# Performance work log

Hardware: AMD Instinct MI355X
Metric: run time of the kernel (lower is better)

The kernel has to match this reference:

```python
import jax, jax.numpy as jnp
import numpy as np


def _rot_mat(thetas, scales):
    # thetas, scales: [bs, g] -> [bs, g, 9, 9] bilinear-interpolation matrices
    bs, g = thetas.shape
    t = thetas.reshape(-1)
    s = scales.reshape(-1)
    x = jnp.cos(t) * s
    y = jnp.sin(t) * s
    yp = -y
    z = jnp.zeros_like(x)
    o = jnp.ones_like(x)
    a = x - y; b = x * y; c = x + y; d = a * c; e = a + c
    ap = x - yp; bp = x * yp; cp = x + yp; dp = ap * cp; ep = ap + cp

    def M(rows):
        # rows: 9 lists of 9 [N]-arrays -> [9, 9, N]
        return jnp.stack([jnp.stack(r, axis=0) for r in rows], axis=0)

    ctr = [z, z, z, z, o, z, z, z, z]

    pb1 = M([
        [a, 1 - a, z, z, z, z, z, z, z],
        [z, 1 - y, y, z, z, z, z, z, z],
        [z, z, a, z, z, 1 - a, z, z, z],
        [y, z, z, 1 - y, z, z, z, z, z],
        ctr,
        [z, z, z, z, z, 1 - y, z, z, y],
        [z, z, z, 1 - a, z, z, a, z, z],
        [z, z, z, z, z, z, y, 1 - y, z],
        [z, z, z, z, z, z, z, 1 - a, a]])
    pb2 = M([
        [a, 1 - a, z, z, z, z, z, z, z],
        [z, x - b, b, z, 1 - c + b, y - b, z, z, z],
        [z, z, a, z, z, 1 - a, z, z, z],
        [b, y - b, z, x - b, 1 - c + b, z, z, z, z],
        ctr,
        [z, z, z, z, 1 - c + b, x - b, z, y - b, b],
        [z, z, z, 1 - a, z, z, a, z, z],
        [z, z, z, y - b, 1 - c + b, z, b, x - b, z],
        [z, z, z, z, z, z, z, 1 - a, a]])
    ps1 = M([
        [d, a - d, z, c - d, 1 - e + d, z, z, z, z],
        [z, x - b, b, z, 1 - c + b, y - b, z, z, z],
        [z, c - d, d, z, 1 - e + d, a - d, z, z, z],
        [b, y - b, z, x - b, 1 - c + b, z, z, z, z],
        ctr,
        [z, z, z, z, 1 - c + b, x - b, z, y - b, b],
        [z, z, z, a - d, 1 - e + d, z, d, c - d, z],
        [z, z, z, y - b, 1 - c + b, z, b, x - b, z],
        [z, z, z, z, 1 - e + d, c - d, z, a - d, d]])
    ps2 = pb2  # identical in the source
    nb1 = M([
        [cp, z, z, 1 - cp, z, z, z, z, z],
        [yp, 1 - yp, z, z, z, z, z, z, z],
        [z, 1 - cp, cp, z, z, z, z, z, z],
        [z, z, z, 1 - yp, z, z, yp, z, z],
        ctr,
        [z, z, yp, z, z, 1 - yp, z, z, z],
        [z, z, z, z, z, z, cp, 1 - cp, z],
        [z, z, z, z, z, z, z, 1 - yp, yp],
        [z, z, z, z, z, 1 - cp, z, z, cp]])
    nb2 = M([
        [cp, z, z, 1 - cp, z, z, z, z, z],
        [bp, x - bp, z, yp - bp, 1 - cp + bp, z, z, z, z],
        [z, 1 - cp, cp, z, z, z, z, z, z],
        [z, z, z, x - bp, 1 - cp + bp, z, bp, yp - bp, z],
        ctr,
        [z, yp - bp, bp, z, 1 - cp + bp, x - bp, z, z, z],
        [z, z, z, z, z, z, cp, 1 - cp, z],
        [z, z, z, z, 1 - cp + bp, yp - bp, z, x - bp, bp],
        [z, z, z, z, z, 1 - cp, z, z, cp]])
    ns1 = M([
        [dp, cp - dp, z, ap - dp, 1 - ep + dp, z, z, z, z],
        [bp, x - bp, z, yp - bp, 1 - cp + bp, z, z, z, z],
        [z, ap - dp, dp, z, 1 - ep + dp, cp - dp, z, z, z],
        [z, yp - bp, bp, z, 1 - cp + bp, x - bp, z, z, z],
        ctr,
        [z, z, z, x - bp, 1 - cp + bp, z, bp, yp - bp, z],
        [z, z, z, cp - dp, 1 - ep + dp, z, dp, ap - dp, z],
        [z, z, z, z, 1 - cp + bp, yp - bp, z, x - bp, bp],
        [z, z, z, z, 1 - ep + dp, ap - dp, z, cp - dp, dp]])
    ns2 = nb2  # mirrors the positive branch where small_2 == big_2

    m_pos = (t >= 0.0)[None, None, :]
    m_big = (s >= 1.0)[None, None, :]
    m_1 = (jnp.abs(t) <= jnp.pi / 4)[None, None, :]
    pos = jnp.where(m_big, jnp.where(m_1, pb1, pb2), jnp.where(m_1, ps1, ps2))
    neg = jnp.where(m_big, jnp.where(m_1, nb1, nb2), jnp.where(m_1, ns1, ns2))
    rot = jnp.where(m_pos, pos, neg)  # [9, 9, bs*g]
    return jnp.transpose(rot, (2, 0, 1)).reshape(bs, g, 9, 9)


def _forward(x, thetas, scales, lambdas, weight):
    # x: [B, Cin, H, W]; weight: [n, Cout, Cin, 3, 3]; thetas/scales/lambdas: [B, n]
    B, Cin, H, W = x.shape
    n, Cout = weight.shape[0], weight.shape[1]
    rot = _rot_mat(thetas, scales) * lambdas[:, :, None, None]  # [B, n, 9, 9]
    w9 = weight.reshape(n, Cout, Cin, 9)
    # per-sample transformed kernel: sum over kernel_number n and source taps j
    w = jnp.einsum('bnij,nocj->bioc', rot, w9)  # [B, 9, Cout, Cin]
    w = jnp.transpose(w, (0, 2, 3, 1)).reshape(B * Cout, Cin, 3, 3)
    xg = x.reshape(1, B * Cin, H, W)
    out = jax.lax.conv_general_dilated(
        xg, w, window_strides=(1, 1), padding=((1, 1), (1, 1)),
        dimension_numbers=('NCHW', 'OIHW', 'NCHW'), feature_group_count=B)
    return out.reshape(B, Cout, H, W)


def setup_inputs() -> dict:
    key = jax.random.key(0)
    ks = jax.random.split(key, 5)
    B, Cin, Cout, H, W, n = 16, 256, 256, 64, 64, 4
    x = jax.random.normal(ks[0], (B, Cin, H, W), dtype=jnp.float32)
    thetas = jax.random.uniform(ks[1], (B, n), minval=-1.2, maxval=1.2, dtype=jnp.float32)
    scales = jax.random.uniform(ks[2], (B, n), minval=0.5, maxval=1.5, dtype=jnp.float32)
    lambdas = jax.nn.softmax(jax.random.normal(ks[3], (B, n), dtype=jnp.float32), axis=-1)
    weight = jax.random.normal(ks[4], (n, Cout, Cin, 3, 3), dtype=jnp.float32) * 0.05
    return {"x": x, "thetas": thetas, "scales": scales, "lambdas": lambdas, "weight": weight}


def reference(x, thetas, scales, lambdas, weight):
    return _forward(x, thetas, scales, lambdas, weight)
```

## Files before the change

### kernel.cpp

```cpp
#include <hip/hip_runtime.h>
#include <cstdint>
#include <cstddef>

typedef unsigned short ushort_t;
typedef __attribute__((ext_vector_type(4))) float f32x4;
typedef __attribute__((ext_vector_type(8))) short s16x8;

#define PI_4F 0.78539816339744830962f

__device__ inline ushort_t f2bf(float f) {
  unsigned int u = __float_as_uint(f);
  u = u + 0x7fffu + ((u >> 16) & 1u);
  return (ushort_t)(u >> 16);
}

__global__ void rot_kernel(const float* __restrict__ thetas, const float* __restrict__ scales,
                           const float* __restrict__ lambdas, float* __restrict__ rot) {
  int tid = threadIdx.x;
  float t = thetas[tid], s = scales[tid], lam = lambdas[tid];
  float xv = cosf(t) * s, yv = sinf(t) * s;
  bool pos = (t >= 0.0f), big = (s >= 1.0f), m1 = (fabsf(t) <= PI_4F);
  float M[81];
#pragma unroll
  for (int i = 0; i < 81; ++i) M[i] = 0.0f;
  M[36 + 4] = 1.0f;
  if (pos) {
    float a = xv - yv, bb = xv * yv, c = xv + yv;
    if (m1 && big) {
      M[0] = a; M[1] = 1 - a;
      M[9 + 1] = 1 - yv; M[9 + 2] = yv;
      M[18 + 2] = a; M[18 + 5] = 1 - a;
      M[27 + 0] = yv; M[27 + 3] = 1 - yv;
      M[45 + 5] = 1 - yv; M[45 + 8] = yv;
      M[54 + 3] = 1 - a; M[54 + 6] = a;
      M[63 + 6] = yv; M[63 + 7] = 1 - yv;
      M[72 + 7] = 1 - a; M[72 + 8] = a;
    } else if (m1) {
      float d = a * c, e = a + c;
      M[0] = d; M[1] = a - d; M[3] = c - d; M[4] = 1 - e + d;
      M[9 + 1] = xv - bb; M[9 + 2] = bb; M[9 + 4] = 1 - c + bb; M[9 + 5] = yv - bb;
      M[18 + 1] = c - d; M[18 + 2] = d; M[18 + 4] = 1 - e + d; M[18 + 5] = a - d;
      M[27 + 0] = bb; M[27 + 1] = yv - bb; M[27 + 3] = xv - bb; M[27 + 4] = 1 - c + bb;
      M[45 + 4] = 1 - c + bb; M[45 + 5] = xv - bb; M[45 + 7] = yv - bb; M[45 + 8] = bb;
      M[54 + 3] = a - d; M[54 + 4] = 1 - e + d; M[54 + 6] = d; M[54 + 7] = c - d;
      M[63 + 3] = yv - bb; M[63 + 4] = 1 - c + bb; M[63 + 6] = bb; M[63 + 7] = xv - bb;
      M[72 + 4] = 1 - e + d; M[72 + 5] = c - d; M[72 + 7] = a - d; M[72 + 8] = d;
    } else {
      M[0] = a; M[1] = 1 - a;
      M[9 + 1] = xv - bb; M[9 + 2] = bb; M[9 + 4] = 1 - c + bb; M[9 + 5] = yv - bb;
      M[18 + 2] = a; M[18 + 5] = 1 - a;
      M[27 + 0] = bb; M[27 + 1] = yv - bb; M[27 + 3] = xv - bb; M[27 + 4] = 1 - c + bb;
      M[45 + 4] = 1 - c + bb; M[45 + 5] = xv - bb; M[45 + 7] = yv - bb; M[45 + 8] = bb;
      M[54 + 3] = 1 - a; M[54 + 6] = a;
      M[63 + 3] = yv - bb; M[63 + 4] = 1 - c + bb; M[63 + 6] = bb; M[63 + 7] = xv - bb;
      M[72 + 7] = 1 - a; M[72 + 8] = a;
    }
  } else {
    float yp = -yv;
    float ap = xv - yp, bp = xv * yp, cp = xv + yp;
    if (m1 && big) {
      M[0] = cp; M[3] = 1 - cp;
      M[9 + 0] = yp; M[9 + 1] = 1 - yp;
      M[18 + 1] = 1 - cp; M[18 + 2] = cp;
      M[27 + 3] = 1 - yp; M[27 + 6] = yp;
      M[45 + 2] = yp; M[45 + 5] = 1 - yp;
      M[54 + 6] = cp; M[54 + 7] = 1 - cp;
      M[63 + 7] = 1 - yp; M[63 + 8] = yp;
      M[72 + 5] = 1 - cp; M[72 + 8] = cp;
    } else if (m1) {
      float dp = ap * cp, ep = ap + cp;
      M[0] = dp; M[1] = cp - dp; M[3] = ap - dp; M[4] = 1 - ep + dp;
      M[9 + 0] = bp; M[9 + 1] = xv - bp; M[9 + 3] = yp - bp; M[9 + 4] = 1 - cp + bp;
      M[18 + 1] = ap - dp; M[18 + 2] = dp; M[18 + 4] = 1 - ep + dp; M[18 + 5] = cp - dp;
      M[27 + 1] = yp - bp; M[27 + 2] = bp; M[27 + 4] = 1 - cp + bp; M[27 + 5] = xv - bp;
      M[45 + 3] = xv - bp; M[45 + 4] = 1 - cp + bp; M[45 + 6] = bp; M[45 + 7] = yp - bp;
      M[54 + 3] = cp - dp; M[54 + 4] = 1 - ep + dp; M[54 + 6] = dp; M[54 + 7] = ap - dp;
      M[63 + 4] = 1 - cp + bp; M[63 + 5] = yp - bp; M[63 + 7] = xv - bp; M[63 + 8] = bp;
      M[72 + 4] = 1 - ep + dp; M[72 + 5] = ap - dp; M[72 + 7] = cp - dp; M[72 + 8] = dp;
    } else {
      M[0] = cp; M[3] = 1 - cp;
      M[9 + 0] = bp; M[9 + 1] = xv - bp; M[9 + 3] = yp - bp; M[9 + 4] = 1 - cp + bp;
      M[18 + 1] = 1 - cp; M[18 + 2] = cp;
      M[27 + 3] = xv - bp; M[27 + 4] = 1 - cp + bp; M[27 + 6] = bp; M[27 + 7] = yp - bp;
      M[45 + 1] = yp - bp; M[45 + 2] = bp; M[45 + 4] = 1 - cp + bp; M[45 + 5] = xv - bp;
      M[54 + 6] = cp; M[54 + 7] = 1 - cp;
      M[63 + 4] = 1 - cp + bp; M[63 + 5] = yp - bp; M[63 + 7] = xv - bp; M[63 + 8] = bp;
      M[72 + 5] = 1 - cp; M[72 + 8] = cp;
    }
  }
  float* r = rot + tid * 81;
#pragma unroll
  for (int i = 0; i < 81; ++i) r[i] = M[i] * lam;
}

__global__ void wt_kernel(const float* __restrict__ weight, const float* __restrict__ rot,
                          ushort_t* __restrict__ wtout) {
  __shared__ float rs[64 * 81];
  const int o = blockIdx.x;
  const int c = threadIdx.x;
  for (int i = threadIdx.x; i < 64 * 81; i += 256) rs[i] = rot[i];
  float wv[4][9];
#pragma unroll
  for (int n = 0; n < 4; ++n) {
    const float* wp = weight + (((size_t)(n * 256 + o)) * 256 + c) * 9;
#pragma unroll
    for (int j = 0; j < 9; ++j) wv[n][j] = wp[j];
  }
  __syncthreads();
  for (int b = 0; b < 16; ++b) {
#pragma unroll
    for (int i = 0; i < 9; ++i) {
      float acc = 0.0f;
#pragma unroll
      for (int n = 0; n < 4; ++n) {
        const float* r = &rs[(b * 4 + n) * 81 + i * 9];
#pragma unroll
        for (int j = 0; j < 9; ++j) acc = fmaf(r[j], wv[n][j], acc);
      }
      wtout[((size_t)((b * 9 + i) * 256 + o)) * 256 + c] = f2bf(acc);
    }
  }
}

__global__ void fill_zero(uint4* __restrict__ p) {
  p[(size_t)blockIdx.x * 256 + threadIdx.x] = make_uint4(0u, 0u, 0u, 0u);
}

__global__ void transpose_kernel(const float* __restrict__ x, ushort_t* __restrict__ xpad) {
  __shared__ float tile[32][33];
  const int b = blockIdx.z, ct = blockIdx.y, st = blockIdx.x;
  const int tx = threadIdx.x & 31, ty = threadIdx.x >> 5;
  const int hw0 = st * 32, c0 = ct * 32;
  const float* xb = x + ((size_t)(b * 256 + c0)) * 4096 + hw0;
#pragma unroll
  for (int j = 0; j < 4; ++j)
    tile[ty + j * 8][tx] = xb[(size_t)(ty + j * 8) * 4096 + tx];
  __syncthreads();
#pragma unroll
  for (int j = 0; j < 4; ++j) {
    int s = ty + j * 8;
    int hw = hw0 + s;
    int h = hw >> 6, w = hw & 63;
    xpad[((size_t)(b * 4356 + (h + 1) * 66 + (w + 1))) * 256 + c0 + tx] = f2bf(tile[tx][s]);
  }
}

__device__ inline void gload16(const ushort_t* g, ushort_t* l) {
  __builtin_amdgcn_global_load_lds(
      (const __attribute__((address_space(1))) unsigned int*)g,
      (__attribute__((address_space(3))) unsigned int*)l, 16, 0, 0);
}

__global__ void conv_kernel(const ushort_t* __restrict__ xpad, const ushort_t* __restrict__ wt,
                            float* __restrict__ out) {
  __shared__ __align__(16) ushort_t As[128 * 32];
  __shared__ __align__(16) ushort_t Bs[128 * 32];
  const int ntile = blockIdx.x;
  const int mtile = blockIdx.y;
  const int b = blockIdx.z;
  const int t = threadIdx.x;
  const int wave = t >> 6, lane = t & 63;
  const int wm = wave & 1, wn = wave >> 1;
  const int lr = lane & 15, lq = lane >> 4;
  const int o0 = mtile * 128, h0 = ntile * 2;

  const ushort_t* wt_b = wt + (size_t)b * 589824;
  const ushort_t* xp_b = xpad + (size_t)b * 1115136;

  const int lrow = t >> 2;
  const int lco = (t & 3) * 8;

  ushort_t* As0 = As + wave * 512;
  ushort_t* As1 = As + 2048 + wave * 512;
  ushort_t* Bs0 = Bs + wave * 512;
  ushort_t* Bs1 = Bs + 2048 + wave * 512;

  f32x4 acc[4][4];
#pragma unroll
  for (int i = 0; i < 4; ++i)
#pragma unroll
    for (int j = 0; j < 4; ++j) acc[i][j] = (f32x4)(0.0f);

  for (int ks = 0; ks < 72; ++ks) {
    const int tap = ks >> 3;
    const int c0 = (ks & 7) << 5;
    const int kh = tap / 3, kw = tap - kh * 3;

    __syncthreads();
    {
      const ushort_t* ga = wt_b + ((size_t)(tap * 256 + o0 + lrow)) * 256 + c0 + lco;
      gload16(ga, As0);
      gload16(ga + 64 * 256, As1);
      const int sp0 = (h0 + kh) * 66 + lrow + kw;
      const ushort_t* gb = xp_b + (size_t)sp0 * 256 + c0 + lco;
      gload16(gb, Bs0);
      gload16(gb + 66 * 256, Bs1);
    }
    asm volatile("s_waitcnt vmcnt(0)" ::: "memory");
    __syncthreads();

    s16x8 af[4], bfr[4];
#pragma unroll
    for (int mi = 0; mi < 4; ++mi)
      af[mi] = *(const s16x8*)(As + ((wm * 64 + mi * 16 + lr) * 32 + lq * 8));
#pragma unroll
    for (int ni = 0; ni < 4; ++ni)
      bfr[ni] = *(const s16x8*)(Bs + ((wn * 64 + ni * 16 + lr) * 32 + lq * 8));
#pragma unroll
    for (int mi = 0; mi < 4; ++mi)
#pragma unroll
      for (int ni = 0; ni < 4; ++ni)
        acc[mi][ni] = __builtin_amdgcn_mfma_f32_16x16x32_bf16(af[mi], bfr[ni], acc[mi][ni], 0, 0, 0);
  }

  float* ob = out + ((size_t)(b * 256 + o0 + wm * 64)) * 4096 + ntile * 128 + wn * 64 + lr;
#pragma unroll
  for (int mi = 0; mi < 4; ++mi)
#pragma unroll
    for (int r = 0; r < 4; ++r) {
      float* orow = ob + (size_t)(mi * 16 + lq * 4 + r) * 4096;
#pragma unroll
      for (int ni = 0; ni < 4; ++ni) orow[ni * 16] = acc[mi][ni][r];
    }
}

extern "C" void kernel_launch(void* const* d_in, const int* in_sizes, int n_in,
                              void* d_out, int out_size, void* d_ws, size_t ws_size,
                              hipStream_t stream) {
  const float* x = (const float*)d_in[0];
  const float* thetas = (const float*)d_in[1];
  const float* scales = (const float*)d_in[2];
  const float* lambdas = (const float*)d_in[3];
  const float* weight = (const float*)d_in[4];
  float* out = (float*)d_out;

  float* rot_ws = (float*)d_ws;
  ushort_t* wt_ws = (ushort_t*)((char*)d_ws + 32768);
  ushort_t* xpad_ws = (ushort_t*)((char*)d_ws + 32768 + 18874368);

  rot_kernel<<<1, 64, 0, stream>>>(thetas, scales, lambdas, rot_ws);
  wt_kernel<<<256, 256, 0, stream>>>(weight, rot_ws, wt_ws);
  fill_zero<<<8712, 256, 0, stream>>>((uint4*)xpad_ws);
  transpose_kernel<<<dim3(128, 8, 16), 256, 0, stream>>>(x, xpad_ws);
  conv_kernel<<<dim3(32, 2, 16), 256, 0, stream>>>(xpad_ws, wt_ws, out);
}
```

Before: 256.3 us.

## Double-buffer conv LDS, swizzle layout, remap blocks per XCD, fuse rot, zero only borders

The conv kernel now double-buffers its LDS tiles, issuing the next k-step's global-to-LDS loads before the current step's MFMAs, and adds an XOR swizzle on the 16-byte column groups to cut LDS bank conflicts. Blocks are remapped onto a 1D grid so each XCD handles a contiguous group of batch/mtile pairs for L2 locality, and launch bounds are added. The rotation-matrix computation is folded into the weight-transform kernel, which removes one launch at the cost of recomputing it in every block. The full padded-buffer memset is replaced with a kernel that zeroes only the border pixels.

```diff
diff --git a/kernel.cpp b/kernel.cpp
--- a/kernel.cpp
+++ b/kernel.cpp
@@ -14,91 +14,91 @@
   return (ushort_t)(u >> 16);
 }
 
-__global__ void rot_kernel(const float* __restrict__ thetas, const float* __restrict__ scales,
-                           const float* __restrict__ lambdas, float* __restrict__ rot) {
-  int tid = threadIdx.x;
-  float t = thetas[tid], s = scales[tid], lam = lambdas[tid];
-  float xv = cosf(t) * s, yv = sinf(t) * s;
-  bool pos = (t >= 0.0f), big = (s >= 1.0f), m1 = (fabsf(t) <= PI_4F);
-  float M[81];
-#pragma unroll
-  for (int i = 0; i < 81; ++i) M[i] = 0.0f;
-  M[36 + 4] = 1.0f;
-  if (pos) {
-    float a = xv - yv, bb = xv * yv, c = xv + yv;
-    if (m1 && big) {
-      M[0] = a; M[1] = 1 - a;
-      M[9 + 1] = 1 - yv; M[9 + 2] = yv;
-      M[18 + 2] = a; M[18 + 5] = 1 - a;
-      M[27 + 0] = yv; M[27 + 3] = 1 - yv;
-      M[45 + 5] = 1 - yv; M[45 + 8] = yv;
-      M[54 + 3] = 1 - a; M[54 + 6] = a;
-      M[63 + 6] = yv; M[63 + 7] = 1 - yv;
-      M[72 + 7] = 1 - a; M[72 + 8] = a;
-    } else if (m1) {
-      float d = a * c, e = a + c;
-      M[0] = d; M[1] = a - d; M[3] = c - d; M[4] = 1 - e + d;
-      M[9 + 1] = xv - bb; M[9 + 2] = bb; M[9 + 4] = 1 - c + bb; M[9 + 5] = yv - bb;
-      M[18 + 1] = c - d; M[18 + 2] = d; M[18 + 4] = 1 - e + d; M[18 + 5] = a - d;
-      M[27 + 0] = bb; M[27 + 1] = yv - bb; M[27 + 3] = xv - bb; M[27 + 4] = 1 - c + bb;
-      M[45 + 4] = 1 - c + bb; M[45 + 5] = xv - bb; M[45 + 7] = yv - bb; M[45 + 8] = bb;
-      M[54 + 3] = a - d; M[54 + 4] = 1 - e + d; M[54 + 6] = d; M[54 + 7] = c - d;
-      M[63 + 3] = yv - bb; M[63 + 4] = 1 - c + bb; M[63 + 6] = bb; M[63 + 7] = xv - bb;
-      M[72 + 4] = 1 - e + d; M[72 + 5] = c - d; M[72 + 7] = a - d; M[72 + 8] = d;
-    } else {
-      M[0] = a; M[1] = 1 - a;
-      M[9 + 1] = xv - bb; M[9 + 2] = bb; M[9 + 4] = 1 - c + bb; M[9 + 5] = yv - bb;
-      M[18 + 2] = a; M[18 + 5] = 1 - a;
-      M[27 + 0] = bb; M[27 + 1] = yv - bb; M[27 + 3] = xv - bb; M[27 + 4] = 1 - c + bb;
-      M[45 + 4] = 1 - c + bb; M[45 + 5] = xv - bb; M[45 + 7] = yv - bb; M[45 + 8] = bb;
-      M[54 + 3] = 1 - a; M[54 + 6] = a;
-      M[63 + 3] = yv - bb; M[63 + 4] = 1 - c + bb; M[63 + 6] = bb; M[63 + 7] = xv - bb;
-      M[72 + 7] = 1 - a; M[72 + 8] = a;
-    }
-  } else {
-    float yp = -yv;
-    float ap = xv - yp, bp = xv * yp, cp = xv + yp;
-    if (m1 && big) {
-      M[0] = cp; M[3] = 1 - cp;
-      M[9 + 0] = yp; M[9 + 1] = 1 - yp;
-      M[18 + 1] = 1 - cp; M[18 + 2] = cp;
-      M[27 + 3] = 1 - yp; M[27 + 6] = yp;
-      M[45 + 2] = yp; M[45 + 5] = 1 - yp;
-      M[54 + 6] = cp; M[54 + 7] = 1 - cp;
-      M[63 + 7] = 1 - yp; M[63 + 8] = yp;
-      M[72 + 5] = 1 - cp; M[72 + 8] = cp;
-    } else if (m1) {
-      float dp = ap * cp, ep = ap + cp;
-      M[0] = dp; M[1] = cp - dp; M[3] = ap - dp; M[4] = 1 - ep + dp;
-      M[9 + 0] = bp; M[9 + 1] = xv - bp; M[9 + 3] = yp - bp; M[9 + 4] = 1 - cp + bp;
-      M[18 + 1] = ap - dp; M[18 + 2] = dp; M[18 + 4] = 1 - ep + dp; M[18 + 5] = cp - dp;
-      M[27 + 1] = yp - bp; M[27 + 2] = bp; M[27 + 4] = 1 - cp + bp; M[27 + 5] = xv - bp;
-      M[45 + 3] = xv - bp; M[45 + 4] = 1 - cp + bp; M[45 + 6] = bp; M[45 + 7] = yp - bp;
-      M[54 + 3] = cp - dp; M[54 + 4] = 1 - ep + dp; M[54 + 6] = dp; M[54 + 7] = ap - dp;
-      M[63 + 4] = 1 - cp + bp; M[63 + 5] = yp - bp; M[63 + 7] = xv - bp; M[63 + 8] = bp;
-      M[72 + 4] = 1 - ep + dp; M[72 + 5] = ap - dp; M[72 + 7] = cp - dp; M[72 + 8] = dp;
-    } else {
-      M[0] = cp; M[3] = 1 - cp;
-      M[9 + 0] = bp; M[9 + 1] = xv - bp; M[9 + 3] = yp - bp; M[9 + 4] = 1 - cp + bp;
-      M[18 + 1] = 1 - cp; M[18 + 2] = cp;
-      M[27 + 3] = xv - bp; M[27 + 4] = 1 - cp + bp; M[27 + 6] = bp; M[27 + 7] = yp - bp;
-      M[45 + 1] = yp - bp; M[45 + 2] = bp; M[45 + 4] = 1 - cp + bp; M[45 + 5] = xv - bp;
-      M[54 + 6] = cp; M[54 + 7] = 1 - cp;
-      M[63 + 4] = 1 - cp + bp; M[63 + 5] = yp - bp; M[63 + 7] = xv - bp; M[63 + 8] = bp;
-      M[72 + 5] = 1 - cp; M[72 + 8] = cp;
-    }
-  }
-  float* r = rot + tid * 81;
-#pragma unroll
-  for (int i = 0; i < 81; ++i) r[i] = M[i] * lam;
-}
-
-__global__ void wt_kernel(const float* __restrict__ weight, const float* __restrict__ rot,
-                          ushort_t* __restrict__ wtout) {
+__global__ void wt_kernel(const float* __restrict__ weight,
+                          const float* __restrict__ thetas, const float* __restrict__ scales,
+                          const float* __restrict__ lambdas, ushort_t* __restrict__ wtout) {
   __shared__ float rs[64 * 81];
   const int o = blockIdx.x;
   const int c = threadIdx.x;
-  for (int i = threadIdx.x; i < 64 * 81; i += 256) rs[i] = rot[i];
+
+  if (threadIdx.x < 64) {
+    int tid = threadIdx.x;
+    float t = thetas[tid], s = scales[tid], lam = lambdas[tid];
+    float xv = cosf(t) * s, yv = sinf(t) * s;
+    bool pos = (t >= 0.0f), big = (s >= 1.0f), m1 = (fabsf(t) <= PI_4F);
+    float M[81];
+#pragma unroll
+    for (int i = 0; i < 81; ++i) M[i] = 0.0f;
+    M[36 + 4] = 1.0f;
+    if (pos) {
+      float a = xv - yv, bb = xv * yv, cc = xv + yv;
+      if (m1 && big) {
+        M[0] = a; M[1] = 1 - a;
+        M[9 + 1] = 1 - yv; M[9 + 2] = yv;
+        M[18 + 2] = a; M[18 + 5] = 1 - a;
+        M[27 + 0] = yv; M[27 + 3] = 1 - yv;
+        M[45 + 5] = 1 - yv; M[45 + 8] = yv;
+        M[54 + 3] = 1 - a; M[54 + 6] = a;
+        M[63 + 6] = yv; M[63 + 7] = 1 - yv;
+        M[72 + 7] = 1 - a; M[72 + 8] = a;
+      } else if (m1) {
+        float d = a * cc, e = a + cc;
+        M[0] = d; M[1] = a - d; M[3] = cc - d; M[4] = 1 - e + d;
+        M[9 + 1] = xv - bb; M[9 + 2] = bb; M[9 + 4] = 1 - cc + bb; M[9 + 5] = yv - bb;
+        M[18 + 1] = cc - d; M[18 + 2] = d; M[18 + 4] = 1 - e + d; M[18 + 5] = a - d;
+        M[27 + 0] = bb; M[27 + 1] = yv - bb; M[27 + 3] = xv - bb; M[27 + 4] = 1 - cc + bb;
+        M[45 + 4] = 1 - cc + bb; M[45 + 5] = xv - bb; M[45 + 7] = yv - bb; M[45 + 8] = bb;
+        M[54 + 3] = a - d; M[54 + 4] = 1 - e + d; M[54 + 6] = d; M[54 + 7] = cc - d;
+        M[63 + 3] = yv - bb; M[63 + 4] = 1 - cc + bb; M[63 + 6] = bb; M[63 + 7] = xv - bb;
+        M[72 + 4] = 1 - e + d; M[72 + 5] = cc - d; M[72 + 7] = a - d; M[72 + 8] = d;
+      } else {
+        M[0] = a; M[1] = 1 - a;
+        M[9 + 1] = xv - bb; M[9 + 2] = bb; M[9 + 4] = 1 - cc + bb; M[9 + 5] = yv - bb;
+        M[18 + 2] = a; M[18 + 5] = 1 - a;
+        M[27 + 0] = bb; M[27 + 1] = yv - bb; M[27 + 3] = xv - bb; M[27 + 4] = 1 - cc + bb;
+        M[45 + 4] = 1 - cc + bb; M[45 + 5] = xv - bb; M[45 + 7] = yv - bb; M[45 + 8] = bb;
+        M[54 + 3] = 1 - a; M[54 + 6] = a;
+        M[63 + 3] = yv - bb; M[63 + 4] = 1 - cc + bb; M[63 + 6] = bb; M[63 + 7] = xv - bb;
+        M[72 + 7] = 1 - a; M[72 + 8] = a;
+      }
+    } else {
+      float yp = -yv;
+      float ap = xv - yp, bp = xv * yp, cp = xv + yp;
+      if (m1 && big) {
+        M[0] = cp; M[3] = 1 - cp;
+        M[9 + 0] = yp; M[9 + 1] = 1 - yp;
+        M[18 + 1] = 1 - cp; M[18 + 2] = cp;
+        M[27 + 3] = 1 - yp; M[27 + 6] = yp;
+        M[45 + 2] = yp; M[45 + 5] = 1 - yp;
+        M[54 + 6] = cp; M[54 + 7] = 1 - cp;
+        M[63 + 7] = 1 - yp; M[63 + 8] = yp;
+        M[72 + 5] = 1 - cp; M[72 + 8] = cp;
+      } else if (m1) {
+        float dp = ap * cp, ep = ap + cp;
+        M[0] = dp; M[1] = cp - dp; M[3] = ap - dp; M[4] = 1 - ep + dp;
+        M[9 + 0] = bp; M[9 + 1] = xv - bp; M[9 + 3] = yp - bp; M[9 + 4] = 1 - cp + bp;
+        M[18 + 1] = ap - dp; M[18 + 2] = dp; M[18 + 4] = 1 - ep + dp; M[18 + 5] = cp - dp;
+        M[27 + 1] = yp - bp; M[27 + 2] = bp; M[27 + 4] = 1 - cp + bp; M[27 + 5] = xv - bp;
+        M[45 + 3] = xv - bp; M[45 + 4] = 1 - cp + bp; M[45 + 6] = bp; M[45 + 7] = yp - bp;
+        M[54 + 3] = cp - dp; M[54 + 4] = 1 - ep + dp; M[54 + 6] = dp; M[54 + 7] = ap - dp;
+        M[63 + 4] = 1 - cp + bp; M[63 + 5] = yp - bp; M[63 + 7] = xv - bp; M[63 + 8] = bp;
+        M[72 + 4] = 1 - ep + dp; M[72 + 5] = ap - dp; M[72 + 7] = cp - dp; M[72 + 8] = dp;
+      } else {
+        M[0] = cp; M[3] = 1 - cp;
+        M[9 + 0] = bp; M[9 + 1] = xv - bp; M[9 + 3] = yp - bp; M[9 + 4] = 1 - cp + bp;
+        M[18 + 1] = 1 - cp; M[18 + 2] = cp;
+        M[27 + 3] = xv - bp; M[27 + 4] = 1 - cp + bp; M[27 + 6] = bp; M[27 + 7] = yp - bp;
+        M[45 + 1] = yp - bp; M[45 + 2] = bp; M[45 + 4] = 1 - cp + bp; M[45 + 5] = xv - bp;
+        M[54 + 6] = cp; M[54 + 7] = 1 - cp;
+        M[63 + 4] = 1 - cp + bp; M[63 + 5] = yp - bp; M[63 + 7] = xv - bp; M[63 + 8] = bp;
+        M[72 + 5] = 1 - cp; M[72 + 8] = cp;
+      }
+    }
+    float* r = rs + tid * 81;
+#pragma unroll
+    for (int i = 0; i < 81; ++i) r[i] = M[i] * lam;
+  }
+
   float wv[4][9];
 #pragma unroll
   for (int n = 0; n < 4; ++n) {
@@ -122,8 +122,15 @@
   }
 }
 
-__global__ void fill_zero(uint4* __restrict__ p) {
-  p[(size_t)blockIdx.x * 256 + threadIdx.x] = make_uint4(0u, 0u, 0u, 0u);
+__global__ void border_zero(ushort_t* __restrict__ xpad) {
+  const int p = blockIdx.x, b = blockIdx.y;
+  int h, w;
+  if (p < 66) { h = 0; w = p; }
+  else if (p < 132) { h = 65; w = p - 66; }
+  else if (p < 196) { w = 0; h = p - 131; }
+  else { w = 65; h = p - 195; }
+  size_t base = ((size_t)(b * 4356 + h * 66 + w)) * 256 + threadIdx.x * 4;
+  *(uint2*)(xpad + base) = make_uint2(0u, 0u);
 }
 
 __global__ void transpose_kernel(const float* __restrict__ x, ushort_t* __restrict__ xpad) {
@@ -151,13 +158,19 @@
       (__attribute__((address_space(3))) unsigned int*)l, 16, 0, 0);
 }
 
-__global__ void conv_kernel(const ushort_t* __restrict__ xpad, const ushort_t* __restrict__ wt,
-                            float* __restrict__ out) {
-  __shared__ __align__(16) ushort_t As[128 * 32];
-  __shared__ __align__(16) ushort_t Bs[128 * 32];
-  const int ntile = blockIdx.x;
-  const int mtile = blockIdx.y;
-  const int b = blockIdx.z;
+__global__ __launch_bounds__(256, 4) void conv_kernel(
+    const ushort_t* __restrict__ xpad, const ushort_t* __restrict__ wt,
+    float* __restrict__ out) {
+  __shared__ __align__(16) ushort_t As[2][128 * 32];
+  __shared__ __align__(16) ushort_t Bs[2][128 * 32];
+
+  const int id = blockIdx.x;
+  const int xcd = id & 7;
+  const int j = id >> 3;
+  const int P = xcd * 4 + (j >> 5);
+  const int b = P >> 1, mtile = P & 1;
+  const int ntile = j & 31;
+
   const int t = threadIdx.x;
   const int wave = t >> 6, lane = t & 63;
   const int wm = wave & 1, wn = wave >> 1;
@@ -168,44 +181,47 @@
   const ushort_t* xp_b = xpad + (size_t)b * 1115136;
 
   const int lrow = t >> 2;
-  const int lco = (t & 3) * 8;
-
-  ushort_t* As0 = As + wave * 512;
-  ushort_t* As1 = As + 2048 + wave * 512;
-  ushort_t* Bs0 = Bs + wave * 512;
-  ushort_t* Bs1 = Bs + 2048 + wave * 512;
+  const int cg8 = (((t & 3) ^ ((t >> 3) & 3)) * 8);
+
+  const int rsw = (lr >> 1) & 3;
+  const int aoff = (wm * 64 + lr) * 32 + (lq ^ rsw) * 8;
+  const int boff = (wn * 64 + lr) * 32 + (lq ^ rsw) * 8;
 
   f32x4 acc[4][4];
 #pragma unroll
   for (int i = 0; i < 4; ++i)
 #pragma unroll
-    for (int j = 0; j < 4; ++j) acc[i][j] = (f32x4)(0.0f);
+    for (int jj = 0; jj < 4; ++jj) acc[i][jj] = (f32x4)(0.0f);
+
+  auto stage = [&](int ks, int buf) {
+    const int tap = ks >> 3;
+    const int c0k = (ks & 7) << 5;
+    const int kh = tap / 3, kw = tap - kh * 3;
+    const ushort_t* ga = wt_b + ((size_t)(tap * 256 + o0 + lrow)) * 256 + c0k + cg8;
+    gload16(ga, &As[buf][wave * 512]);
+    gload16(ga + 64 * 256, &As[buf][2048 + wave * 512]);
+    const ushort_t* gb = xp_b + ((size_t)((h0 + kh) * 66 + lrow + kw)) * 256 + c0k + cg8;
+    gload16(gb, &Bs[buf][wave * 512]);
+    gload16(gb + 66 * 256, &Bs[buf][2048 + wave * 512]);
+  };
+
+  stage(0, 0);
 
   for (int ks = 0; ks < 72; ++ks) {
-    const int tap = ks >> 3;
-    const int c0 = (ks & 7) << 5;
-    const int kh = tap / 3, kw = tap - kh * 3;
-
-    __syncthreads();
-    {
-      const ushort_t* ga = wt_b + ((size_t)(tap * 256 + o0 + lrow)) * 256 + c0 + lco;
-      gload16(ga, As0);
-      gload16(ga + 64 * 256, As1);
-      const int sp0 = (h0 + kh) * 66 + lrow + kw;
-      const ushort_t* gb = xp_b + (size_t)sp0 * 256 + c0 + lco;
-      gload16(gb, Bs0);
-      gload16(gb + 66 * 256, Bs1);
-    }
+    const int buf = ks & 1;
     asm volatile("s_waitcnt vmcnt(0)" ::: "memory");
     __syncthreads();
-
+    if (ks < 71) stage(ks + 1, buf ^ 1);
+
+    const ushort_t* Ab = &As[buf][0];
+    const ushort_t* Bb = &Bs[buf][0];
     s16x8 af[4], bfr[4];
 #pragma unroll
     for (int mi = 0; mi < 4; ++mi)
-      af[mi] = *(const s16x8*)(As + ((wm * 64 + mi * 16 + lr) * 32 + lq * 8));
+      af[mi] = *(const s16x8*)(Ab + aoff + mi * 512);
 #pragma unroll
     for (int ni = 0; ni < 4; ++ni)
-      bfr[ni] = *(const s16x8*)(Bs + ((wn * 64 + ni * 16 + lr) * 32 + lq * 8));
+      bfr[ni] = *(const s16x8*)(Bb + boff + ni * 512);
 #pragma unroll
     for (int mi = 0; mi < 4; ++mi)
 #pragma unroll
@@ -234,13 +250,11 @@
   const float* weight = (const float*)d_in[4];
   float* out = (float*)d_out;
 
-  float* rot_ws = (float*)d_ws;
-  ushort_t* wt_ws = (ushort_t*)((char*)d_ws + 32768);
-  ushort_t* xpad_ws = (ushort_t*)((char*)d_ws + 32768 + 18874368);
-
-  rot_kernel<<<1, 64, 0, stream>>>(thetas, scales, lambdas, rot_ws);
-  wt_kernel<<<256, 256, 0, stream>>>(weight, rot_ws, wt_ws);
-  fill_zero<<<8712, 256, 0, stream>>>((uint4*)xpad_ws);
+  ushort_t* wt_ws = (ushort_t*)d_ws;
+  ushort_t* xpad_ws = (ushort_t*)((char*)d_ws + 18874368);
+
+  wt_kernel<<<256, 256, 0, stream>>>(weight, thetas, scales, lambdas, wt_ws);
+  border_zero<<<dim3(260, 16), 64, 0, stream>>>(xpad_ws);
   transpose_kernel<<<dim3(128, 8, 16), 256, 0, stream>>>(x, xpad_ws);
-  conv_kernel<<<dim3(32, 2, 16), 256, 0, stream>>>(xpad_ws, wt_ws, out);
-}
+  conv_kernel<<<1024, 256, 0, stream>>>(xpad_ws, wt_ws, out);
+}
```

Measured after the change: 241.9 us. -5.6%, faster.

## Restructure conv pipeline, border-only zeroing, wider transpose, XCD-aware grid

Applied to the files above, without the earlier changes.

The conv kernel now uses a 3-stage LDS ring buffer with asynchronous global-to-LDS prefetch two steps ahead. Each block covers all 256 output channels for a 2-row tile, and the LDS layout is XOR-swizzled to reduce bank conflicts. Blocks are mapped so each XCD handles two batches, which improves L2 locality. The full zero-fill of the padded buffer is replaced by zeroing only the border, the transpose uses 64x64 tiles stored as bf16 with vectorized writes, and wt_kernel is split over batch groups and reads rot from global memory instead of LDS. The trade-off is higher register and LDS use per block, and the hand-placed waitcnt counts are fragile.

```diff
diff --git a/kernel.cpp b/kernel.cpp
--- a/kernel.cpp
+++ b/kernel.cpp
@@ -95,10 +95,8 @@
 
 __global__ void wt_kernel(const float* __restrict__ weight, const float* __restrict__ rot,
                           ushort_t* __restrict__ wtout) {
-  __shared__ float rs[64 * 81];
-  const int o = blockIdx.x;
+  const int o = blockIdx.x, bg = blockIdx.y;
   const int c = threadIdx.x;
-  for (int i = threadIdx.x; i < 64 * 81; i += 256) rs[i] = rot[i];
   float wv[4][9];
 #pragma unroll
   for (int n = 0; n < 4; ++n) {
@@ -106,14 +104,15 @@
 #pragma unroll
     for (int j = 0; j < 9; ++j) wv[n][j] = wp[j];
   }
-  __syncthreads();
-  for (int b = 0; b < 16; ++b) {
+#pragma unroll
+  for (int bl = 0; bl < 4; ++bl) {
+    const int b = bg * 4 + bl;
 #pragma unroll
     for (int i = 0; i < 9; ++i) {
       float acc = 0.0f;
 #pragma unroll
       for (int n = 0; n < 4; ++n) {
-        const float* r = &rs[(b * 4 + n) * 81 + i * 9];
+        const float* r = rot + (b * 4 + n) * 81 + i * 9;
 #pragma unroll
         for (int j = 0; j < 9; ++j) acc = fmaf(r[j], wv[n][j], acc);
       }
@@ -122,26 +121,36 @@
   }
 }
 
-__global__ void fill_zero(uint4* __restrict__ p) {
-  p[(size_t)blockIdx.x * 256 + threadIdx.x] = make_uint4(0u, 0u, 0u, 0u);
+__global__ void border_zero(ushort_t* __restrict__ xpad) {
+  const int p = blockIdx.x, b = blockIdx.y;
+  int h, w;
+  if (p < 66) { h = 0; w = p; }
+  else if (p < 132) { h = 65; w = p - 66; }
+  else if (p < 196) { w = 0; h = p - 131; }
+  else { w = 65; h = p - 195; }
+  size_t base = ((size_t)(b * 4356 + h * 66 + w)) * 256 + threadIdx.x * 4;
+  *(uint2*)(xpad + base) = make_uint2(0u, 0u);
 }
 
 __global__ void transpose_kernel(const float* __restrict__ x, ushort_t* __restrict__ xpad) {
-  __shared__ float tile[32][33];
+  __shared__ ushort_t tile[64][65];
   const int b = blockIdx.z, ct = blockIdx.y, st = blockIdx.x;
-  const int tx = threadIdx.x & 31, ty = threadIdx.x >> 5;
-  const int hw0 = st * 32, c0 = ct * 32;
-  const float* xb = x + ((size_t)(b * 256 + c0)) * 4096 + hw0;
-#pragma unroll
-  for (int j = 0; j < 4; ++j)
-    tile[ty + j * 8][tx] = xb[(size_t)(ty + j * 8) * 4096 + tx];
+  const int t = threadIdx.x;
+  const int l = t & 63, wv = t >> 6;
+  const int c0 = ct * 64;
+  const float* xb = x + ((size_t)(b * 256 + c0)) * 4096 + st * 64;
+#pragma unroll
+  for (int k = 0; k < 16; ++k) {
+    int c_l = wv + 4 * k;
+    tile[l][c_l] = f2bf(xb[(size_t)c_l * 4096 + l]);
+  }
   __syncthreads();
-#pragma unroll
-  for (int j = 0; j < 4; ++j) {
-    int s = ty + j * 8;
-    int hw = hw0 + s;
-    int h = hw >> 6, w = hw & 63;
-    xpad[((size_t)(b * 4356 + (h + 1) * 66 + (w + 1))) * 256 + c0 + tx] = f2bf(tile[tx][s]);
+  const int hw_l0 = t >> 4, c4 = (t & 15) * 4;
+#pragma unroll
+  for (int k = 0; k < 4; ++k) {
+    int w = hw_l0 + 16 * k;
+    uint2 v = *(const uint2*)&tile[w][c4];
+    *(uint2*)&xpad[((size_t)(b * 4356 + (st + 1) * 66 + (w + 1))) * 256 + c0 + c4] = v;
   }
 }
 
@@ -151,76 +160,96 @@
       (__attribute__((address_space(3))) unsigned int*)l, 16, 0, 0);
 }
 
-__global__ void conv_kernel(const ushort_t* __restrict__ xpad, const ushort_t* __restrict__ wt,
-                            float* __restrict__ out) {
-  __shared__ __align__(16) ushort_t As[128 * 32];
-  __shared__ __align__(16) ushort_t Bs[128 * 32];
-  const int ntile = blockIdx.x;
-  const int mtile = blockIdx.y;
-  const int b = blockIdx.z;
+__global__ __launch_bounds__(256, 2) void conv_kernel(
+    const ushort_t* __restrict__ xpad, const ushort_t* __restrict__ wt,
+    float* __restrict__ out) {
+  __shared__ __align__(16) ushort_t As[3][256 * 32];
+  __shared__ __align__(16) ushort_t Bs[3][128 * 32];
+
+  const int id = blockIdx.x;
+  const int xcd = id & 7;
+  const int j = id >> 3;
+  const int b = xcd * 2 + (j >> 5);
+  const int ntile = j & 31;
+
   const int t = threadIdx.x;
   const int wave = t >> 6, lane = t & 63;
   const int wm = wave & 1, wn = wave >> 1;
   const int lr = lane & 15, lq = lane >> 4;
-  const int o0 = mtile * 128, h0 = ntile * 2;
+  const int h0 = ntile * 2;
 
   const ushort_t* wt_b = wt + (size_t)b * 589824;
   const ushort_t* xp_b = xpad + (size_t)b * 1115136;
 
   const int lrow = t >> 2;
-  const int lco = (t & 3) * 8;
-
-  ushort_t* As0 = As + wave * 512;
-  ushort_t* As1 = As + 2048 + wave * 512;
-  ushort_t* Bs0 = Bs + wave * 512;
-  ushort_t* Bs1 = Bs + 2048 + wave * 512;
-
-  f32x4 acc[4][4];
-#pragma unroll
-  for (int i = 0; i < 4; ++i)
-#pragma unroll
-    for (int j = 0; j < 4; ++j) acc[i][j] = (f32x4)(0.0f);
-
-  for (int ks = 0; ks < 72; ++ks) {
+  const int cg8 = (((t & 3) ^ ((t >> 3) & 3)) * 8);
+
+  const int rsw = (lr >> 1) & 3;
+  const int aoff = (wm * 128 + lr) * 32 + ((lq ^ rsw) * 8);
+  const int boff = (wn * 64 + lr) * 32 + ((lq ^ rsw) * 8);
+
+  f32x4 acc[8][4];
+#pragma unroll
+  for (int i = 0; i < 8; ++i)
+#pragma unroll
+    for (int jj = 0; jj < 4; ++jj) acc[i][jj] = (f32x4)(0.0f);
+
+  auto stage = [&](int ks, int buf) {
     const int tap = ks >> 3;
-    const int c0 = (ks & 7) << 5;
+    const int c0k = (ks & 7) << 5;
     const int kh = tap / 3, kw = tap - kh * 3;
-
-    __syncthreads();
-    {
-      const ushort_t* ga = wt_b + ((size_t)(tap * 256 + o0 + lrow)) * 256 + c0 + lco;
-      gload16(ga, As0);
-      gload16(ga + 64 * 256, As1);
-      const int sp0 = (h0 + kh) * 66 + lrow + kw;
-      const ushort_t* gb = xp_b + (size_t)sp0 * 256 + c0 + lco;
-      gload16(gb, Bs0);
-      gload16(gb + 66 * 256, Bs1);
-    }
-    asm volatile("s_waitcnt vmcnt(0)" ::: "memory");
-    __syncthreads();
-
-    s16x8 af[4], bfr[4];
-#pragma unroll
-    for (int mi = 0; mi < 4; ++mi)
-      af[mi] = *(const s16x8*)(As + ((wm * 64 + mi * 16 + lr) * 32 + lq * 8));
+    const ushort_t* ga = wt_b + ((size_t)(tap * 256 + lrow)) * 256 + c0k + cg8;
+    ushort_t* Ad = &As[buf][wave * 512];
+#pragma unroll
+    for (int a = 0; a < 4; ++a) gload16(ga + (size_t)a * 64 * 256, Ad + a * 2048);
+    const ushort_t* gb = xp_b + ((size_t)((h0 + kh) * 66 + lrow + kw)) * 256 + c0k + cg8;
+    ushort_t* Bd = &Bs[buf][wave * 512];
+    gload16(gb, Bd);
+    gload16(gb + 66 * 256, Bd + 2048);
+  };
+
+  auto compute = [&](int buf) {
+    const ushort_t* Ab = &As[buf][0];
+    const ushort_t* Bb = &Bs[buf][0];
+    s16x8 bfr[4];
 #pragma unroll
     for (int ni = 0; ni < 4; ++ni)
-      bfr[ni] = *(const s16x8*)(Bs + ((wn * 64 + ni * 16 + lr) * 32 + lq * 8));
-#pragma unroll
-    for (int mi = 0; mi < 4; ++mi)
+      bfr[ni] = *(const s16x8*)(Bb + boff + ni * 512);
+#pragma unroll
+    for (int ms = 0; ms < 8; ++ms) {
+      s16x8 af = *(const s16x8*)(Ab + aoff + ms * 512);
 #pragma unroll
       for (int ni = 0; ni < 4; ++ni)
-        acc[mi][ni] = __builtin_amdgcn_mfma_f32_16x16x32_bf16(af[mi], bfr[ni], acc[mi][ni], 0, 0, 0);
-  }
-
-  float* ob = out + ((size_t)(b * 256 + o0 + wm * 64)) * 4096 + ntile * 128 + wn * 64 + lr;
-#pragma unroll
-  for (int mi = 0; mi < 4; ++mi)
+        acc[ms][ni] = __builtin_amdgcn_mfma_f32_16x16x32_bf16(af, bfr[ni], acc[ms][ni], 0, 0, 0);
+    }
+  };
+
+  stage(0, 0);
+  stage(1, 1);
+
+  int bc = 0;
+  for (int ks = 0; ks < 71; ++ks) {
+    asm volatile("s_waitcnt vmcnt(6)" ::: "memory");
+    asm volatile("s_barrier" ::: "memory");
+    if (ks < 70) {
+      int bp = (bc == 0) ? 2 : bc - 1;
+      stage(ks + 2, bp);
+    }
+    compute(bc);
+    bc = (bc == 2) ? 0 : bc + 1;
+  }
+  asm volatile("s_waitcnt vmcnt(0)" ::: "memory");
+  asm volatile("s_barrier" ::: "memory");
+  compute(bc);
+
+  float* ob = out + ((size_t)(b * 256 + wm * 128)) * 4096 + ntile * 128 + wn * 64 + lr;
+#pragma unroll
+  for (int ms = 0; ms < 8; ++ms)
 #pragma unroll
     for (int r = 0; r < 4; ++r) {
-      float* orow = ob + (size_t)(mi * 16 + lq * 4 + r) * 4096;
-#pragma unroll
-      for (int ni = 0; ni < 4; ++ni) orow[ni * 16] = acc[mi][ni][r];
+      float* orow = ob + (size_t)(ms * 16 + lq * 4 + r) * 4096;
+#pragma unroll
+      for (int ni = 0; ni < 4; ++ni) orow[ni * 16] = acc[ms][ni][r];
     }
 }
 
@@ -239,8 +268,8 @@
   ushort_t* xpad_ws = (ushort_t*)((char*)d_ws + 32768 + 18874368);
 
   rot_kernel<<<1, 64, 0, stream>>>(thetas, scales, lambdas, rot_ws);
-  wt_kernel<<<256, 256, 0, stream>>>(weight, rot_ws, wt_ws);
-  fill_zero<<<8712, 256, 0, stream>>>((uint4*)xpad_ws);
-  transpose_kernel<<<dim3(128, 8, 16), 256, 0, stream>>>(x, xpad_ws);
-  conv_kernel<<<dim3(32, 2, 16), 256, 0, stream>>>(xpad_ws, wt_ws, out);
-}
+  wt_kernel<<<dim3(256, 4), 256, 0, stream>>>(weight, rot_ws, wt_ws);
+  border_zero<<<dim3(260, 16), 64, 0, stream>>>(xpad_ws);
+  transpose_kernel<<<dim3(64, 4, 16), 256, 0, stream>>>(x, xpad_ws);
+  conv_kernel<<<512, 256, 0, stream>>>(xpad_ws, wt_ws, out);
+}
```

Measured after the change: 241.4 us. -5.8%, faster.
